# Performance work log

Hardware: AMD Instinct MI355X
Metric: run time of the kernel (lower is better)

Reference implementation:

```python
import jax, jax.numpy as jnp
import numpy as np
from jax import lax

K = 3          # spline order
G = 5          # grid intervals
R0, R1 = -4.0, 4.0  # grid_range
IN, HID, OUT = 32, 128, 16
BATCH, SEQ = 256, 512


def make_grid(n_in):
    # extended knot vector: G+2K+1 knots per input, uniform spacing h
    h = (R1 - R0) / G
    knots = R0 + h * jnp.arange(-K, G + K + 1, dtype=jnp.float32)  # [G+2K+1]
    return jnp.broadcast_to(knots, (n_in, G + 2 * K + 1))


def b_splines(x, grid):
    # Cox-de Boor recursion. x: [B, n], grid: [n, G+2K+1] -> basis [B, n, G+K]
    xg = x[..., None]
    B = ((xg >= grid[:, :-1]) & (xg < grid[:, 1:])).astype(x.dtype)
    for d in range(1, K + 1):
        B = ((xg - grid[:, :-(d + 1)]) / (grid[:, d:-1] - grid[:, :-(d + 1)]) * B[..., :-1]
             + (grid[:, d + 1:] - xg) / (grid[:, d + 1:] - grid[:, 1:-d]) * B[..., 1:])
    return B


def kan_layer(x, coef, scale_base, scale_sp, grid):
    # y[b,o] = sum_i scale_base[i,o]*silu(x[b,i]) + scale_sp[i,o]*spline_io(x[b,i])
    base = jax.nn.silu(x)                               # [B, n_in]
    Bsp = b_splines(x, grid)                            # [B, n_in, G+K]
    spline = jnp.einsum('bik,iok->bio', Bsp, coef)      # [B, n_in, n_out]
    return (jnp.einsum('bi,io->bo', base, scale_base)
            + jnp.einsum('bio,io->bo', spline, scale_sp))


def setup_inputs() -> dict:
    key = jax.random.key(0)
    ks = jax.random.split(key, 7)
    x = jax.random.normal(ks[0], (BATCH, SEQ, IN), dtype=jnp.float32)
    coef1 = jax.random.normal(ks[1], (IN + HID, HID, G + K), dtype=jnp.float32) * 0.1
    sb1 = jax.random.normal(ks[2], (IN + HID, HID), dtype=jnp.float32) * 0.05
    sp1 = jax.random.normal(ks[3], (IN + HID, HID), dtype=jnp.float32) * 0.05
    coef2 = jax.random.normal(ks[4], (HID, OUT, G + K), dtype=jnp.float32) * 0.1
    sb2 = jax.random.normal(ks[5], (HID, OUT), dtype=jnp.float32) * 0.05
    sp2 = jax.random.normal(ks[6], (HID, OUT), dtype=jnp.float32) * 0.05
    return {"x": x, "coef1": coef1, "sb1": sb1, "sp1": sp1,
            "coef2": coef2, "sb2": sb2, "sp2": sp2}


def reference(x, coef1, sb1, sp1, coef2, sb2, sp2):
    grid1 = make_grid(IN + HID)
    grid2 = make_grid(HID)

    def step(h, x_t):
        combined = jnp.concatenate([x_t, h], axis=1)        # [B, IN+HID]
        h_new = kan_layer(combined, coef1, sb1, sp1, grid1)  # [B, HID]
        out_t = kan_layer(h_new, coef2, sb2, sp2, grid2)     # [B, OUT]
        return h_new, out_t

    h0 = jnp.zeros((x.shape[0], HID), dtype=x.dtype)
    _, outs = lax.scan(step, h0, jnp.swapaxes(x, 0, 1))  # outs: [T, B, OUT]
    # original stacks all timestep outputs then returns outputs[:, -1, :]
    return outs[-1]
```

## Files before the change

### kernel.cpp

```cpp
#include <hip/hip_runtime.h>
#include <hip/hip_bf16.h>

#define NIN 32
#define NHID 128
#define NOUT 16
#define NIN1 160
#define SEQT 512
#define NB 256
#define SEGI 40

#if defined(__has_builtin)
#if __has_builtin(__builtin_amdgcn_fdot2_f32_bf16)
#define HAVE_DOT2BF 1
#endif
#endif
#ifndef HAVE_DOT2BF
#define HAVE_DOT2BF 0
#endif

__device__ __forceinline__ unsigned int f2bfbits(float f) {
    unsigned int u = __float_as_uint(f);
    return (u + 0x7fffu + ((u >> 16) & 1u)) >> 16;
}
__device__ __forceinline__ unsigned int packbf(float lo, float hi) {
    return f2bfbits(lo) | (f2bfbits(hi) << 16);
}

#if HAVE_DOT2BF
typedef __bf16 bf16x2 __attribute__((ext_vector_type(2)));
__device__ __forceinline__ float dot2w(unsigned int a, unsigned int b, float c) {
    return __builtin_amdgcn_fdot2_f32_bf16(__builtin_bit_cast(bf16x2, a),
                                           __builtin_bit_cast(bf16x2, b), c, false);
}
#else
__device__ __forceinline__ float dot2w(unsigned int a, unsigned int b, float c) {
    float alo = __uint_as_float(a << 16), ahi = __uint_as_float(a & 0xffff0000u);
    float blo = __uint_as_float(b << 16), bhi = __uint_as_float(b & 0xffff0000u);
    return __builtin_fmaf(ahi, bhi, __builtin_fmaf(alo, blo, c));
}
#endif

__device__ __forceinline__ void spline_feat(float c, float* out4, int* jst) {
    const float t0 = -8.8f, hh = 1.6f;
    int m0 = (int)floorf((c - t0) / hh);
    bool valid = (m0 >= 0) && (m0 <= 10);
    float v0 = 1.f, v1 = 0.f, v2 = 0.f, v3 = 0.f;
    #pragma unroll
    for (int d = 1; d <= 3; ++d) {
        float inv = 1.f / (d * hh);
        float nv[4];
        float pv[4] = {v0, v1, v2, v3};
        #pragma unroll
        for (int r = 3; r >= 0; --r) {
            if (r > d) { nv[r] = 0.f; continue; }
            int m = m0 - d + r;
            float tm = t0 + hh * (float)m;
            float left  = (r >= 1) ? pv[r-1] : 0.f;
            float right = (r <= d-1) ? pv[r] : 0.f;
            nv[r] = ((c - tm) * left + (tm + hh * (float)(d+1) - c) * right) * inv;
        }
        v0 = nv[0]; v1 = nv[1]; v2 = nv[2]; v3 = nv[3];
    }
    float v[4] = {v0, v1, v2, v3};
    int jb = m0 - 3;
    int js = jb < 0 ? 0 : (jb > 4 ? 4 : jb);
    int sh = js - jb;
    #pragma unroll
    for (int r = 0; r < 4; ++r) {
        int rs = r + sh;
        out4[r] = (valid && rs >= 0 && rs <= 3) ? v[rs] : 0.f;
    }
    *jst = js;
}

__global__ __launch_bounds__(512, 2)
void kan_seq(const float* __restrict__ x,
             const float* __restrict__ coef1,
             const float* __restrict__ sb1,
             const float* __restrict__ sp1,
             const float* __restrict__ coef2,
             const float* __restrict__ sb2,
             const float* __restrict__ sp2,
             float* __restrict__ out)
{
    __shared__ __align__(16) unsigned int Fb[NIN1][4];
    __shared__ float Fsil[NIN1];
    __shared__ float red[4][NHID];
    __shared__ float Hf[NHID][9];

    const int tid  = threadIdx.x;
    const int b    = blockIdx.x;
    const int o    = tid & 127;
    const int seg  = tid >> 7;
    const int i0   = seg * SEGI;
    const int lane = tid & 63;

    unsigned int cw[SEGI][4];
    unsigned int swp[SEGI / 2];
    #pragma unroll
    for (int ii = 0; ii < SEGI; ++ii) {
        const float4* cp = (const float4*)(coef1 + (size_t)((i0 + ii) * NHID + o) * 8);
        float sp = sp1[(i0 + ii) * NHID + o];
        float4 a = cp[0], c = cp[1];
        cw[ii][0] = packbf(sp * a.x, sp * a.y);
        cw[ii][1] = packbf(sp * a.z, sp * a.w);
        cw[ii][2] = packbf(sp * c.x, sp * c.y);
        cw[ii][3] = packbf(sp * c.z, sp * c.w);
    }
    #pragma unroll
    for (int p = 0; p < SEGI / 2; ++p)
        swp[p] = packbf(sb1[(i0 + 2 * p) * NHID + o], sb1[(i0 + 2 * p + 1) * NHID + o]);

    ((float*)red)[tid] = 0.f;
    float xv = (tid < NIN) ? x[(size_t)b * SEQT * NIN + tid] : 0.f;
    __syncthreads();

    for (int t = 0; t < SEQT; ++t) {
        if (tid < NIN1) {
            float c;
            if (tid < NIN) c = xv;
            else {
                int hi = tid - NIN;
                c = red[0][hi] + red[1][hi] + red[2][hi] + red[3][hi];
            }
            float sil = c / (1.f + __expf(-c));
            float b4[4]; int js;
            spline_feat(c, b4, &js);
            float e[8];
            #pragma unroll
            for (int k = 0; k < 8; ++k) {
                int d = k - js;
                e[k] = (d >= 0 && d < 4) ? b4[d] : 0.f;
            }
            uint4 pk;
            pk.x = packbf(e[0], e[1]); pk.y = packbf(e[2], e[3]);
            pk.z = packbf(e[4], e[5]); pk.w = packbf(e[6], e[7]);
            *(uint4*)&Fb[tid][0] = pk;
            Fsil[tid] = sil;
        }
        if (tid < NIN) {
            int tn = (t + 1 < SEQT) ? (t + 1) : t;
            xv = x[((size_t)b * SEQT + tn) * NIN + tid];
        }
        __syncthreads();

        float vsil = Fsil[i0 + (lane < SEGI ? lane : 0)];
        float ac0 = 0.f, ac1 = 0.f, ac2 = 0.f, ac3 = 0.f;
        #pragma unroll
        for (int p = 0; p < SEGI / 2; ++p) {
            unsigned int sbp = swp[p];
            float sb_lo = __uint_as_float(sbp << 16);
            float sb_hi = __uint_as_float(sbp & 0xffff0000u);
            {
                const int ii = 2 * p;
                float sl = __int_as_float(__builtin_amdgcn_readlane(__float_as_int(vsil), ii));
                uint4 bb = *(const uint4*)&Fb[i0 + ii][0];
                ac0 = __builtin_fmaf(sl, sb_lo, ac0);
                ac0 = dot2w(bb.x, cw[ii][0], ac0);
                ac1 = dot2w(bb.y, cw[ii][1], ac1);
                ac2 = dot2w(bb.z, cw[ii][2], ac2);
                ac3 = dot2w(bb.w, cw[ii][3], ac3);
            }
            {
                const int ii = 2 * p + 1;
                float sl = __int_as_float(__builtin_amdgcn_readlane(__float_as_int(vsil), ii));
                uint4 bb = *(const uint4*)&Fb[i0 + ii][0];
                ac1 = __builtin_fmaf(sl, sb_hi, ac1);
                ac0 = dot2w(bb.x, cw[ii][0], ac0);
                ac1 = dot2w(bb.y, cw[ii][1], ac1);
                ac2 = dot2w(bb.z, cw[ii][2], ac2);
                ac3 = dot2w(bb.w, cw[ii][3], ac3);
            }
        }
        red[seg][o] = (ac0 + ac1) + (ac2 + ac3);
        __syncthreads();
    }

    if (tid < NHID) {
        float c = red[0][tid] + red[1][tid] + red[2][tid] + red[3][tid];
        float sil = c / (1.f + __expf(-c));
        float b4[4]; int js;
        spline_feat(c, b4, &js);
        #pragma unroll
        for (int k = 0; k < 8; ++k) {
            int d = k - js;
            Hf[tid][k] = (d >= 0 && d < 4) ? b4[d] : 0.f;
        }
        Hf[tid][8] = sil;
    }
    __syncthreads();
    if (tid < 128) {
        int o2 = tid & 15, isg = tid >> 4;
        float acc = 0.f;
        for (int q = 0; q < 16; ++q) {
            int i = isg * 16 + q;
            const float* c2 = coef2 + (size_t)(i * NOUT + o2) * 8;
            float s = 0.f;
            #pragma unroll
            for (int k = 0; k < 8; ++k) s += Hf[i][k] * c2[k];
            acc += Hf[i][8] * sb2[i * NOUT + o2] + sp2[i * NOUT + o2] * s;
        }
        ((float*)red)[isg * 16 + o2] = acc;
    }
    __syncthreads();
    if (tid < NOUT) {
        float a = 0.f;
        #pragma unroll
        for (int g = 0; g < 8; ++g) a += ((float*)red)[g * 16 + tid];
        out[(size_t)b * NOUT + tid] = a;
    }
}

extern "C" void kernel_launch(void* const* d_in, const int* in_sizes, int n_in,
                              void* d_out, int out_size, void* d_ws, size_t ws_size,
                              hipStream_t stream) {
    kan_seq<<<NB, 512, 0, stream>>>(
        (const float*)d_in[0], (const float*)d_in[1], (const float*)d_in[2],
        (const float*)d_in[3], (const float*)d_in[4], (const float*)d_in[5],
        (const float*)d_in[6], (float*)d_out);
}
```

Measured before the change: 1.084 ms.

## Halve block to 256 threads, split weights between registers and LDS, use fp16 dot2

The per-block thread count drops from 512 to 256, and each thread now covers 80 inputs instead of 40. The first 46 inputs' scaled coefficients stay in registers and the remaining 34 are staged in shared memory. Spline features move to fp16 and are broadcast via readlane instead of per-iteration LDS loads, and the sb1*silu term is folded into fp16 dot2 calls. The aim is to halve the cross-segment reduction and synchronization cost per timestep. In exchange each thread does more serial work, and the fp16 round-toward-zero conversion changes precision.

Result: slower. 2.128 ms (+96.3%).

```diff
diff --git a/kernel.cpp b/kernel.cpp
--- a/kernel.cpp
+++ b/kernel.cpp
@@ -7,38 +7,6 @@
 #define NIN1 160
 #define SEQT 512
 #define NB 256
-#define SEGI 40
-
-#if defined(__has_builtin)
-#if __has_builtin(__builtin_amdgcn_fdot2_f32_bf16)
-#define HAVE_DOT2BF 1
-#endif
-#endif
-#ifndef HAVE_DOT2BF
-#define HAVE_DOT2BF 0
-#endif
-
-__device__ __forceinline__ unsigned int f2bfbits(float f) {
-    unsigned int u = __float_as_uint(f);
-    return (u + 0x7fffu + ((u >> 16) & 1u)) >> 16;
-}
-__device__ __forceinline__ unsigned int packbf(float lo, float hi) {
-    return f2bfbits(lo) | (f2bfbits(hi) << 16);
-}
-
-#if HAVE_DOT2BF
-typedef __bf16 bf16x2 __attribute__((ext_vector_type(2)));
-__device__ __forceinline__ float dot2w(unsigned int a, unsigned int b, float c) {
-    return __builtin_amdgcn_fdot2_f32_bf16(__builtin_bit_cast(bf16x2, a),
-                                           __builtin_bit_cast(bf16x2, b), c, false);
-}
-#else
-__device__ __forceinline__ float dot2w(unsigned int a, unsigned int b, float c) {
-    float alo = __uint_as_float(a << 16), ahi = __uint_as_float(a & 0xffff0000u);
-    float blo = __uint_as_float(b << 16), bhi = __uint_as_float(b & 0xffff0000u);
-    return __builtin_fmaf(ahi, bhi, __builtin_fmaf(alo, blo, c));
-}
-#endif
 
 __device__ __forceinline__ void spline_feat(float c, float* out4, int* jst) {
     const float t0 = -8.8f, hh = 1.6f;
@@ -73,45 +41,113 @@
     *jst = js;
 }
 
-__global__ __launch_bounds__(512, 2)
-void kan_seq(const float* __restrict__ x,
-             const float* __restrict__ coef1,
-             const float* __restrict__ sb1,
-             const float* __restrict__ sp1,
-             const float* __restrict__ coef2,
-             const float* __restrict__ sb2,
-             const float* __restrict__ sp2,
-             float* __restrict__ out)
+__device__ __forceinline__ float fsilu(float c) {
+    return c * __builtin_amdgcn_rcpf(1.f + __expf(-c));
+}
+
+__device__ __forceinline__ unsigned RL(unsigned v, int lane) {
+    return (unsigned)__builtin_amdgcn_readlane((int)v, lane);
+}
+
+typedef _Float16 h2 __attribute__((ext_vector_type(2)));
+__device__ __forceinline__ unsigned pk2(float a, float b) {
+    return __builtin_bit_cast(unsigned, __builtin_amdgcn_cvt_pkrtz(a, b));
+}
+
+#if defined(__has_builtin)
+#if __has_builtin(__builtin_amdgcn_fdot2)
+#define HAVE_FDOT2 1
+#endif
+#endif
+#ifndef HAVE_FDOT2
+#define HAVE_FDOT2 0
+#endif
+
+#if HAVE_FDOT2
+__device__ __forceinline__ float dot2h(unsigned a, unsigned b, float c) {
+    return __builtin_amdgcn_fdot2(__builtin_bit_cast(h2, a),
+                                  __builtin_bit_cast(h2, b), c, false);
+}
+#else
+__device__ __forceinline__ float dot2h(unsigned a, unsigned b, float c) {
+    h2 ha = __builtin_bit_cast(h2, a), hb = __builtin_bit_cast(h2, b);
+    return fmaf((float)ha[1], (float)hb[1], fmaf((float)ha[0], (float)hb[0], c));
+}
+#endif
+
+#define PW 0
+#define PS 34816
+#define PF 39168
+#define PP 39808
+#define PR 39888
+#define PTOT 40144
+
+__device__ __forceinline__ unsigned fr(uint4 vA, uint2 vB, int r, int c) {
+    if (r < 64) {
+        unsigned x = (c == 0) ? vA.x : (c == 1) ? vA.y : (c == 2) ? vA.z : vA.w;
+        return RL(x, r);
+    } else {
+        int f = 4 * (r - 64) + c;
+        return RL((f & 1) ? vB.y : vB.x, f >> 1);
+    }
+}
+
+__attribute__((amdgpu_num_vgpr(256)))
+__global__ void __launch_bounds__(256)
+kan_res(const float* __restrict__ x,
+        const float* __restrict__ coef1,
+        const float* __restrict__ sb1,
+        const float* __restrict__ sp1,
+        const float* __restrict__ coef2,
+        const float* __restrict__ sb2,
+        const float* __restrict__ sp2,
+        float* __restrict__ out)
 {
-    __shared__ __align__(16) unsigned int Fb[NIN1][4];
-    __shared__ float Fsil[NIN1];
-    __shared__ float red[4][NHID];
-    __shared__ float Hf[NHID][9];
+    __shared__ __align__(16) unsigned pool[PTOT];
+    float* redf = (float*)&pool[PR];
 
     const int tid  = threadIdx.x;
     const int b    = blockIdx.x;
     const int o    = tid & 127;
     const int seg  = tid >> 7;
-    const int i0   = seg * SEGI;
     const int lane = tid & 63;
 
-    unsigned int cw[SEGI][4];
-    unsigned int swp[SEGI / 2];
+    for (int p = tid; p < 68 * 128; p += 256) {
+        int s = p >> 7, oo = p & 127;
+        int sg = s >= 34, li = s - 34 * sg;
+        int i = sg * 80 + 46 + li;
+        const float4* cp = (const float4*)(coef1 + ((size_t)i * 128 + oo) * 8);
+        float sp = sp1[i * 128 + oo];
+        float4 a = cp[0], c = cp[1];
+        *(uint4*)&pool[PW + p * 4] =
+            make_uint4(pk2(sp * a.x, sp * a.y), pk2(sp * a.z, sp * a.w),
+                       pk2(sp * c.x, sp * c.y), pk2(sp * c.z, sp * c.w));
+    }
+    for (int p = tid; p < 34 * 128; p += 256) {
+        int q = p >> 7, oo = p & 127;
+        int sg = q >= 17, qq = q - 17 * sg;
+        int iA = sg * 80 + 46 + 2 * qq;
+        pool[PS + p] = pk2(sb1[iA * 128 + oo], sb1[(iA + 1) * 128 + oo]);
+    }
+
+    uint4 wreg[46];
+    unsigned sbw[23];
     #pragma unroll
-    for (int ii = 0; ii < SEGI; ++ii) {
-        const float4* cp = (const float4*)(coef1 + (size_t)((i0 + ii) * NHID + o) * 8);
-        float sp = sp1[(i0 + ii) * NHID + o];
-        float4 a = cp[0], c = cp[1];
-        cw[ii][0] = packbf(sp * a.x, sp * a.y);
-        cw[ii][1] = packbf(sp * a.z, sp * a.w);
-        cw[ii][2] = packbf(sp * c.x, sp * c.y);
-        cw[ii][3] = packbf(sp * c.z, sp * c.w);
-    }
-    #pragma unroll
-    for (int p = 0; p < SEGI / 2; ++p)
-        swp[p] = packbf(sb1[(i0 + 2 * p) * NHID + o], sb1[(i0 + 2 * p + 1) * NHID + o]);
-
-    ((float*)red)[tid] = 0.f;
+    for (int p = 0; p < 23; ++p) {
+        int iA = seg * 80 + 2 * p;
+        size_t ba = ((size_t)iA * 128 + o) * 8;
+        const float4* ca = (const float4*)(coef1 + ba);
+        const float4* cb = (const float4*)(coef1 + ba + 1024);
+        float sA = sp1[iA * 128 + o], sB = sp1[(iA + 1) * 128 + o];
+        float4 a0 = ca[0], a1 = ca[1], b0 = cb[0], b1 = cb[1];
+        wreg[2 * p]     = make_uint4(pk2(sA * a0.x, sA * a0.y), pk2(sA * a0.z, sA * a0.w),
+                                     pk2(sA * a1.x, sA * a1.y), pk2(sA * a1.z, sA * a1.w));
+        wreg[2 * p + 1] = make_uint4(pk2(sB * b0.x, sB * b0.y), pk2(sB * b0.z, sB * b0.w),
+                                     pk2(sB * b1.x, sB * b1.y), pk2(sB * b1.z, sB * b1.w));
+        sbw[p] = pk2(sb1[iA * 128 + o], sb1[(iA + 1) * 128 + o]);
+    }
+
+    redf[tid] = 0.f;
     float xv = (tid < NIN) ? x[(size_t)b * SEQT * NIN + tid] : 0.f;
     __syncthreads();
 
@@ -119,11 +155,8 @@
         if (tid < NIN1) {
             float c;
             if (tid < NIN) c = xv;
-            else {
-                int hi = tid - NIN;
-                c = red[0][hi] + red[1][hi] + red[2][hi] + red[3][hi];
-            }
-            float sil = c / (1.f + __expf(-c));
+            else { int hi = tid - NIN; c = redf[hi] + redf[128 + hi]; }
+            float sil = fsilu(c);
             float b4[4]; int js;
             spline_feat(c, b4, &js);
             float e[8];
@@ -132,11 +165,11 @@
                 int d = k - js;
                 e[k] = (d >= 0 && d < 4) ? b4[d] : 0.f;
             }
-            uint4 pk;
-            pk.x = packbf(e[0], e[1]); pk.y = packbf(e[2], e[3]);
-            pk.z = packbf(e[4], e[5]); pk.w = packbf(e[6], e[7]);
-            *(uint4*)&Fb[tid][0] = pk;
-            Fsil[tid] = sil;
+            int sg = tid >= 80, r = tid - 80 * sg;
+            *(uint4*)&pool[PF + sg * 320 + r * 4] =
+                make_uint4(pk2(e[0], e[1]), pk2(e[2], e[3]),
+                           pk2(e[4], e[5]), pk2(e[6], e[7]));
+            ((unsigned short*)&pool[PP])[tid] = (unsigned short)(pk2(sil, 0.f) & 0xffffu);
         }
         if (tid < NIN) {
             int tn = (t + 1 < SEQT) ? (t + 1) : t;
@@ -144,49 +177,57 @@
         }
         __syncthreads();
 
-        float vsil = Fsil[i0 + (lane < SEGI ? lane : 0)];
+        uint4 vA = *(const uint4*)&pool[PF + seg * 320 + lane * 4];
+        uint2 vB = make_uint2(0, 0);
+        if (lane < 32) vB = *(const uint2*)&pool[PF + seg * 320 + 256 + lane * 2];
+        unsigned vS = pool[PP + seg * 40 + (lane < 40 ? lane : 0)];
+
         float ac0 = 0.f, ac1 = 0.f, ac2 = 0.f, ac3 = 0.f;
         #pragma unroll
-        for (int p = 0; p < SEGI / 2; ++p) {
-            unsigned int sbp = swp[p];
-            float sb_lo = __uint_as_float(sbp << 16);
-            float sb_hi = __uint_as_float(sbp & 0xffff0000u);
-            {
-                const int ii = 2 * p;
-                float sl = __int_as_float(__builtin_amdgcn_readlane(__float_as_int(vsil), ii));
-                uint4 bb = *(const uint4*)&Fb[i0 + ii][0];
-                ac0 = __builtin_fmaf(sl, sb_lo, ac0);
-                ac0 = dot2w(bb.x, cw[ii][0], ac0);
-                ac1 = dot2w(bb.y, cw[ii][1], ac1);
-                ac2 = dot2w(bb.z, cw[ii][2], ac2);
-                ac3 = dot2w(bb.w, cw[ii][3], ac3);
-            }
-            {
-                const int ii = 2 * p + 1;
-                float sl = __int_as_float(__builtin_amdgcn_readlane(__float_as_int(vsil), ii));
-                uint4 bb = *(const uint4*)&Fb[i0 + ii][0];
-                ac1 = __builtin_fmaf(sl, sb_hi, ac1);
-                ac0 = dot2w(bb.x, cw[ii][0], ac0);
-                ac1 = dot2w(bb.y, cw[ii][1], ac1);
-                ac2 = dot2w(bb.z, cw[ii][2], ac2);
-                ac3 = dot2w(bb.w, cw[ii][3], ac3);
-            }
-        }
-        red[seg][o] = (ac0 + ac1) + (ac2 + ac3);
+        for (int p = 0; p < 23; ++p) {
+            uint4 WA = wreg[2 * p], WB = wreg[2 * p + 1];
+            ac0 = dot2h(fr(vA, vB, 2 * p, 0), WA.x, ac0);
+            ac1 = dot2h(fr(vA, vB, 2 * p, 1), WA.y, ac1);
+            ac2 = dot2h(fr(vA, vB, 2 * p, 2), WA.z, ac2);
+            ac3 = dot2h(fr(vA, vB, 2 * p, 3), WA.w, ac3);
+            ac0 = dot2h(fr(vA, vB, 2 * p + 1, 0), WB.x, ac0);
+            ac1 = dot2h(fr(vA, vB, 2 * p + 1, 1), WB.y, ac1);
+            ac2 = dot2h(fr(vA, vB, 2 * p + 1, 2), WB.z, ac2);
+            ac3 = dot2h(fr(vA, vB, 2 * p + 1, 3), WB.w, ac3);
+            ac0 = dot2h(RL(vS, p), sbw[p], ac0);
+        }
+        #pragma unroll
+        for (int q = 0; q < 17; ++q) {
+            int s0 = ((seg * 34 + 2 * q) << 7) + o;
+            uint4 wa = *(const uint4*)&pool[PW + s0 * 4];
+            uint4 wb = *(const uint4*)&pool[PW + s0 * 4 + 512];
+            unsigned sbq = pool[PS + ((seg * 17 + q) << 7) + o];
+            ac0 = dot2h(fr(vA, vB, 46 + 2 * q, 0), wa.x, ac0);
+            ac1 = dot2h(fr(vA, vB, 46 + 2 * q, 1), wa.y, ac1);
+            ac2 = dot2h(fr(vA, vB, 46 + 2 * q, 2), wa.z, ac2);
+            ac3 = dot2h(fr(vA, vB, 46 + 2 * q, 3), wa.w, ac3);
+            ac0 = dot2h(fr(vA, vB, 47 + 2 * q, 0), wb.x, ac0);
+            ac1 = dot2h(fr(vA, vB, 47 + 2 * q, 1), wb.y, ac1);
+            ac2 = dot2h(fr(vA, vB, 47 + 2 * q, 2), wb.z, ac2);
+            ac3 = dot2h(fr(vA, vB, 47 + 2 * q, 3), wb.w, ac3);
+            ac0 = dot2h(RL(vS, 23 + q), sbq, ac0);
+        }
+        redf[seg * 128 + o] = (ac0 + ac1) + (ac2 + ac3);
         __syncthreads();
     }
 
+    float* Hf = (float*)pool;
     if (tid < NHID) {
-        float c = red[0][tid] + red[1][tid] + red[2][tid] + red[3][tid];
-        float sil = c / (1.f + __expf(-c));
+        float c = redf[tid] + redf[128 + tid];
+        float sil = fsilu(c);
         float b4[4]; int js;
         spline_feat(c, b4, &js);
         #pragma unroll
         for (int k = 0; k < 8; ++k) {
             int d = k - js;
-            Hf[tid][k] = (d >= 0 && d < 4) ? b4[d] : 0.f;
-        }
-        Hf[tid][8] = sil;
+            Hf[tid * 9 + k] = (d >= 0 && d < 4) ? b4[d] : 0.f;
+        }
+        Hf[tid * 9 + 8] = sil;
     }
     __syncthreads();
     if (tid < 128) {
@@ -197,16 +238,16 @@
             const float* c2 = coef2 + (size_t)(i * NOUT + o2) * 8;
             float s = 0.f;
             #pragma unroll
-            for (int k = 0; k < 8; ++k) s += Hf[i][k] * c2[k];
-            acc += Hf[i][8] * sb2[i * NOUT + o2] + sp2[i * NOUT + o2] * s;
-        }
-        ((float*)red)[isg * 16 + o2] = acc;
+            for (int k = 0; k < 8; ++k) s += Hf[i * 9 + k] * c2[k];
+            acc += Hf[i * 9 + 8] * sb2[i * NOUT + o2] + sp2[i * NOUT + o2] * s;
+        }
+        redf[tid] = acc;
     }
     __syncthreads();
     if (tid < NOUT) {
         float a = 0.f;
         #pragma unroll
-        for (int g = 0; g < 8; ++g) a += ((float*)red)[g * 16 + tid];
+        for (int g = 0; g < 8; ++g) a += redf[g * 16 + tid];
         out[(size_t)b * NOUT + tid] = a;
     }
 }
@@ -214,7 +255,7 @@
 extern "C" void kernel_launch(void* const* d_in, const int* in_sizes, int n_in,
                               void* d_out, int out_size, void* d_ws, size_t ws_size,
                               hipStream_t stream) {
-    kan_seq<<<NB, 512, 0, stream>>>(
+    kan_res<<<NB, 256, 0, stream>>>(
         (const float*)d_in[0], (const float*)d_in[1], (const float*)d_in[2],
         (const float*)d_in[3], (const float*)d_in[4], (const float*)d_in[5],
         (const float*)d_in[6], (float*)d_out);
```
